# Performance work log

Measured on AMD Instinct MI355X. Metric: run time of the kernel, lower is better.

## Reference

```python
import jax, jax.numpy as jnp
import numpy as np

S, D = 4096, 512


def setup_inputs() -> dict:
    key = jax.random.key(0)
    ks = jax.random.split(key, 10)
    names = ['x', 'w_ql', 'w_kl', 'w_qr', 'w_kr', 'w_qg', 'w_kg', 'w_qloc', 'w_kloc', 'w_v']
    shapes = [(S, D)] + [(D, D)] * 9
    scale = [1.0] + [float(np.sqrt(2.0 / (D + D)))] * 9  # xavier-ish for weights
    return {n: jax.random.normal(k, sh, dtype=jnp.float32) * s
            for n, k, sh, s in zip(names, ks, shapes, scale)}


def reference(x, w_ql, w_kl, w_qr, w_kr, w_qg, w_kg, w_qloc, w_kloc, w_v):
    # x: [S, D]
    s, d = x.shape
    norm = jnp.sqrt(jnp.asarray(d, x.dtype))
    # strict upper triangle (j > i) is masked for the left boundary,
    # strict lower triangle (i > j) for the right boundary
    mask_up = jnp.triu(jnp.ones((s, s), dtype=bool), k=1)

    ql, kl = x @ w_ql, x @ w_kl
    qr, kr = x @ w_qr, x @ w_kr

    neg_inf = jnp.asarray(-jnp.inf, x.dtype)
    left_scores = jnp.where(mask_up, neg_inf, ql @ kl.T) / norm            # [S,S]
    left_boundary = jax.nn.softmax(left_scores, axis=1)
    right_scores = jnp.where(mask_up.T, neg_inf, qr @ kr.T) / norm
    right_boundary = jax.nn.softmax(right_scores, axis=1)

    # left_boundary @ triu(ones)  == forward cumsum along columns
    # right_boundary @ tril(ones) == reverse cumsum along columns
    left_cdf = jnp.cumsum(left_boundary, axis=1)
    right_cdf = jnp.cumsum(right_boundary[:, ::-1], axis=1)[:, ::-1]
    att_mask = left_cdf * right_cdf                                        # [S,S]

    s_glb = (x @ w_qg) @ (x @ w_kg).T                                      # [S,S]
    s_loc = ((x @ w_qloc) @ (x @ w_kloc).T) * att_mask                     # additive local path
    score = (s_glb + s_loc) / norm

    att_weight = jax.nn.softmax(score, axis=1)
    att_output = att_weight @ (x @ w_v)                                    # [S,D]
    return att_output, att_weight
```

## Files before the change

### kernel.cpp

```cpp
#include <hip/hip_runtime.h>


#define SS 4096
#define DD 512
#define INV_NORM 0.04419417382415922f

typedef _Float16 f16;
typedef f16 f16x8 __attribute__((ext_vector_type(8)));
typedef f16 f16x4 __attribute__((ext_vector_type(4)));
typedef float f32x4 __attribute__((ext_vector_type(4)));

#define GAS __attribute__((address_space(1)))
#define LAS __attribute__((address_space(3)))

__device__ __forceinline__ void ldsdma16(const void* g, void* l) {
  __builtin_amdgcn_global_load_lds((const GAS void*)g, (LAS void*)l, 16, 0, 0);
}

__device__ __forceinline__ void stage16(const f16* __restrict__ src, int ldk, f16* lds, int k0) {
  const int tid  = threadIdx.x;
  const int lane = tid & 63;
  const int wv   = tid >> 6;
  const int rb   = wv * 8 + (lane >> 3);
  const int cs   = lane & 7;
#pragma unroll
  for (int c = 0; c < 4; ++c) {
    const int r = c * 32 + rb;
    const int q = cs ^ (r & 7);
    ldsdma16(src + (size_t)r * ldk + k0 + q * 8, lds + c * 2048 + wv * 512);
  }
}

__device__ __forceinline__ f16x8 fragld(const f16* lds, int r0, int qb) {
  const int lane = threadIdx.x & 63;
  const int r = r0 + (lane & 15);
  const int q = (qb + (lane >> 4)) ^ (r & 7);
  return *(const f16x8*)(lds + r * 64 + q * 8);
}

__device__ __forceinline__ void mma64(const f16* As, const f16* Bs, f32x4 acc[2][8]) {
  const int wv = threadIdx.x >> 6;
#pragma unroll
  for (int ks = 0; ks < 2; ++ks) {
    const f16x8 a0 = fragld(As, wv * 32,      ks * 4);
    const f16x8 a1 = fragld(As, wv * 32 + 16, ks * 4);
#pragma unroll
    for (int j = 0; j < 8; ++j) {
      const f16x8 b = fragld(Bs, j * 16, ks * 4);
      acc[0][j] = __builtin_amdgcn_mfma_f32_16x16x32_f16(a0, b, acc[0][j], 0, 0, 0);
      acc[1][j] = __builtin_amdgcn_mfma_f32_16x16x32_f16(a1, b, acc[1][j], 0, 0, 0);
    }
  }
}

__global__ void k_cvt_x(const float* __restrict__ x, f16* __restrict__ xh) {
  const size_t i = ((size_t)blockIdx.x * 256 + threadIdx.x) * 4;
  const float4 f = *(const float4*)(x + i);
  f16x4 h = { (f16)f.x, (f16)f.y, (f16)f.z, (f16)f.w };
  *(f16x4*)(xh + i) = h;
}

__global__ void k_trw(const float* w0, const float* w1, const float* w2, const float* w3,
                      const float* w4, const float* w5, const float* w6, const float* w7,
                      const float* w8, f16* __restrict__ wt) {
  const float* srcs[9] = {w0, w1, w2, w3, w4, w5, w6, w7, w8};
  const float* src = srcs[blockIdx.z];
  f16* dst = wt + (size_t)blockIdx.z * DD * DD;
  __shared__ float t[32][33];
  const int n0 = blockIdx.x * 32, k0 = blockIdx.y * 32;
  const int tx = threadIdx.x, ty = threadIdx.y;
#pragma unroll
  for (int i = 0; i < 32; i += 8)
    t[ty + i][tx] = src[(size_t)(k0 + ty + i) * DD + n0 + tx];
  __syncthreads();
#pragma unroll
  for (int i = 0; i < 32; i += 8)
    dst[(size_t)(n0 + ty + i) * DD + k0 + tx] = (f16)t[tx][ty + i];
}

__global__ void k_trv(const f16* __restrict__ v, f16* __restrict__ vt) {
  __shared__ f16 t[32][33];
  const int n0 = blockIdx.x * 32, s0 = blockIdx.y * 32;
  const int tx = threadIdx.x, ty = threadIdx.y;
#pragma unroll
  for (int i = 0; i < 32; i += 8)
    t[ty + i][tx] = v[(size_t)(s0 + ty + i) * DD + n0 + tx];
  __syncthreads();
#pragma unroll
  for (int i = 0; i < 32; i += 8)
    vt[(size_t)(n0 + ty + i) * SS + s0 + tx] = t[tx][ty + i];
}

__global__ __launch_bounds__(256, 2) void k_proj(const f16* __restrict__ xh,
                                                 const f16* __restrict__ wt,
                                                 f16* __restrict__ proj) {
  __shared__ __align__(16) f16 As[8192];
  __shared__ __align__(16) f16 Bs[8192];
  const int z = blockIdx.z;
  const f16* B = wt + (size_t)z * DD * DD;
  f16* C = proj + (size_t)z * SS * DD;
  const int R0 = blockIdx.y * 128, C0 = blockIdx.x * 128;
  f32x4 acc[2][8];
#pragma unroll
  for (int i = 0; i < 2; ++i)
#pragma unroll
    for (int j = 0; j < 8; ++j) acc[i][j] = (f32x4){0.f, 0.f, 0.f, 0.f};
  for (int kb = 0; kb < DD / 64; ++kb) {
    __syncthreads();
    stage16(xh + (size_t)R0 * DD, DD, As, kb * 64);
    stage16(B  + (size_t)C0 * DD, DD, Bs, kb * 64);
    __syncthreads();
    mma64(As, Bs, acc);
  }
  const int lane = threadIdx.x & 63, wv = threadIdx.x >> 6;
  const int mm = lane & 15, quad = lane >> 4;
#pragma unroll
  for (int i = 0; i < 2; ++i)
#pragma unroll
    for (int j = 0; j < 8; ++j)
#pragma unroll
      for (int r = 0; r < 4; ++r)
        C[(size_t)(R0 + wv * 32 + i * 16 + quad * 4 + r) * DD + C0 + j * 16 + mm] =
            (f16)acc[i][j][r];
}

__global__ __launch_bounds__(256, 2) void k_bnd(const f16* __restrict__ proj,
                                                f16* __restrict__ eL,
                                                f16* __restrict__ eR) {
  const int jt = blockIdx.x, rbk = blockIdx.y, dir = blockIdx.z;
  if (dir == 0 ? (jt > rbk) : (jt < rbk)) return;
  __shared__ __align__(16) f16 As[8192];
  __shared__ __align__(16) f16 Bs[8192];
  const f16* q  = proj + (size_t)(dir ? 2 : 0) * SS * DD;
  const f16* kp = proj + (size_t)(dir ? 3 : 1) * SS * DD;
  const int R0 = rbk * 128, C0 = jt * 128;
  f32x4 acc[2][8];
#pragma unroll
  for (int i = 0; i < 2; ++i)
#pragma unroll
    for (int j = 0; j < 8; ++j) acc[i][j] = (f32x4){0.f, 0.f, 0.f, 0.f};
  for (int kb = 0; kb < DD / 64; ++kb) {
    __syncthreads();
    stage16(q  + (size_t)R0 * DD, DD, As, kb * 64);
    stage16(kp + (size_t)C0 * DD, DD, Bs, kb * 64);
    __syncthreads();
    mma64(As, Bs, acc);
  }
  const int lane = threadIdx.x & 63, wv = threadIdx.x >> 6;
  const int mm = lane & 15, quad = lane >> 4;
  const bool diag = (jt == rbk);
  f16* outp = dir ? eR : eL;
#pragma unroll
  for (int i = 0; i < 2; ++i)
#pragma unroll
    for (int r = 0; r < 4; ++r) {
      const int rl = wv * 32 + i * 16 + quad * 4 + r;
#pragma unroll
      for (int j = 0; j < 8; ++j) {
        const int cl = j * 16 + mm;
        const float sc = acc[i][j][r] * INV_NORM;
        const bool bad = diag && (dir ? (cl < rl) : (cl > rl));
        const float e = bad ? 0.f : __expf(sc);
        outp[(size_t)(R0 + rl) * SS + (C0 + cl)] = (f16)e;
      }
    }
}

__global__ __launch_bounds__(1024) void k_cumsum(f16* __restrict__ eL,
                                                 const f16* __restrict__ eR) {
  const int i = blockIdx.x;
  const int tid = threadIdx.x, lane = tid & 63, wv = tid >> 6;
  __shared__ float wsL[16], wsR[16];
  const int j0 = tid * 4;

  const f16x4 hl = *(const f16x4*)(eL + (size_t)i * SS + j0);
  float pl[4];
#pragma unroll
  for (int u = 0; u < 4; ++u) pl[u] = (j0 + u <= i) ? (float)hl[u] : 0.f;
#pragma unroll
  for (int u = 1; u < 4; ++u) pl[u] += pl[u - 1];
  const float Tl = pl[3];
  float sl = Tl;
#pragma unroll
  for (int d = 1; d < 64; d <<= 1) {
    const float o = __shfl_up(sl, (unsigned)d, 64);
    if (lane >= d) sl += o;
  }
  if (lane == 63) wsL[wv] = sl;

  const f16x4 hr = *(const f16x4*)(eR + (size_t)i * SS + j0);
  float rr[4], pr[4];
#pragma unroll
  for (int u = 0; u < 4; ++u) rr[u] = (j0 + u >= i) ? (float)hr[u] : 0.f;
  pr[0] = rr[0];
#pragma unroll
  for (int u = 1; u < 4; ++u) pr[u] = pr[u - 1] + rr[u];
  const float Tr = pr[3];
  float sr = Tr;
#pragma unroll
  for (int d = 1; d < 64; d <<= 1) {
    const float o = __shfl_up(sr, (unsigned)d, 64);
    if (lane >= d) sr += o;
  }
  if (lane == 63) wsR[wv] = sr;

  __syncthreads();
  float offL = 0.f, totL = 0.f, offR = 0.f, totR = 0.f;
#pragma unroll
  for (int ww = 0; ww < 16; ++ww) {
    const float a = wsL[ww], b = wsR[ww];
    if (ww < wv) { offL += a; offR += b; }
    totL += a; totR += b;
  }
  const float exL = offL + sl - Tl;
  const float exR = offR + sr - Tr;
  const float invL = 1.f / totL, invR = 1.f / totR;

  f16x4 out;
#pragma unroll
  for (int u = 0; u < 4; ++u) {
    const int j = j0 + u;
    const float cdfL = (exL + pl[u]) * invL;
    const float pre  = exR + pr[u];
    const float cdfR = (totR - pre + rr[u]) * invR;
    const float m = (j < i) ? cdfL : ((j > i) ? cdfR : 1.f);
    out[u] = (f16)m;
  }
  *(f16x4*)(eL + (size_t)i * SS + j0) = out;
}

__global__ __launch_bounds__(256, 2) void k_score(const f16* __restrict__ proj,
                                                  const f16* __restrict__ mask,
                                                  f16* __restrict__ ehalf,
                                                  float* __restrict__ lsc) {
  __shared__ __align__(16) f16 Ag[8192];
  __shared__ __align__(16) f16 Bg[8192];
  __shared__ __align__(16) f16 Al[8192];
  __shared__ __align__(16) f16 Bl[8192];
  const int jt = blockIdx.x, rbk = blockIdx.y;
  const f16* qg = proj + (size_t)4 * SS * DD;
  const f16* kg = proj + (size_t)5 * SS * DD;
  const f16* ql = proj + (size_t)6 * SS * DD;
  const f16* kl = proj + (size_t)7 * SS * DD;
  const int R0 = rbk * 128, C0 = jt * 128;
  f32x4 ag[2][8], al[2][8];
#pragma unroll
  for (int i = 0; i < 2; ++i)
#pragma unroll
    for (int j = 0; j < 8; ++j) {
      ag[i][j] = (f32x4){0.f, 0.f, 0.f, 0.f};
      al[i][j] = (f32x4){0.f, 0.f, 0.f, 0.f};
    }
  for (int kb = 0; kb < DD / 64; ++kb) {
    __syncthreads();
    stage16(qg + (size_t)R0 * DD, DD, Ag, kb * 64);
    stage16(kg + (size_t)C0 * DD, DD, Bg, kb * 64);
    stage16(ql + (size_t)R0 * DD, DD, Al, kb * 64);
    stage16(kl + (size_t)C0 * DD, DD, Bl, kb * 64);
    __syncthreads();
    mma64(Ag, Bg, ag);
    mma64(Al, Bl, al);
  }
  const int lane = threadIdx.x & 63, wv = threadIdx.x >> 6;
  const int mm = lane & 15, quad = lane >> 4;
  float ls[2][4];
#pragma unroll
  for (int i = 0; i < 2; ++i)
#pragma unroll
    for (int r = 0; r < 4; ++r) ls[i][r] = 0.f;
#pragma unroll
  for (int i = 0; i < 2; ++i)
#pragma unroll
    for (int r = 0; r < 4; ++r) {
      const int rg = R0 + wv * 32 + i * 16 + quad * 4 + r;
#pragma unroll
      for (int j = 0; j < 8; ++j) {
        const int cg = C0 + j * 16 + mm;
        const float mk = (float)mask[(size_t)rg * SS + cg];
        const float scv = (ag[i][j][r] + al[i][j][r] * mk) * INV_NORM;
        const float e = __expf(scv);
        ehalf[(size_t)rg * SS + cg] = (f16)e;
        ls[i][r] += e;
      }
    }
#pragma unroll
  for (int d = 1; d < 16; d <<= 1)
#pragma unroll
    for (int i = 0; i < 2; ++i)
#pragma unroll
      for (int r = 0; r < 4; ++r)
        ls[i][r] += __shfl_xor(ls[i][r], d, 64);
  if (mm == 0) {
#pragma unroll
    for (int i = 0; i < 2; ++i)
#pragma unroll
      for (int r = 0; r < 4; ++r)
        atomicAdd(&lsc[R0 + wv * 32 + i * 16 + quad * 4 + r], ls[i][r]);
  }
}

__global__ void k_norm(const f16* __restrict__ ehalf, const float* __restrict__ lsc,
                       float* __restrict__ outw) {
  const size_t idx = ((size_t)blockIdx.x * 256 + threadIdx.x) * 8;
  const int row = (int)(idx >> 12);
  const float inv = 1.f / lsc[row];
  const f16x8 h = *(const f16x8*)(ehalf + idx);
  float4 a = { (float)h[0] * inv, (float)h[1] * inv, (float)h[2] * inv, (float)h[3] * inv };
  float4 b = { (float)h[4] * inv, (float)h[5] * inv, (float)h[6] * inv, (float)h[7] * inv };
  *(float4*)(outw + idx) = a;
  *(float4*)(outw + idx + 4) = b;
}

__global__ __launch_bounds__(256, 2) void k_pv(const f16* __restrict__ ehalf,
                                               const f16* __restrict__ vt,
                                               float* __restrict__ part) {
  __shared__ __align__(16) f16 As[8192];
  __shared__ __align__(16) f16 Bs[8192];
  const int C0 = blockIdx.x * 128, R0 = blockIdx.y * 128, zk = blockIdx.z;
  f32x4 acc[2][8];
#pragma unroll
  for (int i = 0; i < 2; ++i)
#pragma unroll
    for (int j = 0; j < 8; ++j) acc[i][j] = (f32x4){0.f, 0.f, 0.f, 0.f};
  for (int kb = 0; kb < 16; ++kb) {
    const int k0 = zk * 1024 + kb * 64;
    __syncthreads();
    stage16(ehalf + (size_t)R0 * SS, SS, As, k0);
    stage16(vt    + (size_t)C0 * SS, SS, Bs, k0);
    __syncthreads();
    mma64(As, Bs, acc);
  }
  const int lane = threadIdx.x & 63, wv = threadIdx.x >> 6;
  const int mm = lane & 15, quad = lane >> 4;
  float* P = part + (size_t)zk * SS * DD;
#pragma unroll
  for (int i = 0; i < 2; ++i)
#pragma unroll
    for (int j = 0; j < 8; ++j)
#pragma unroll
      for (int r = 0; r < 4; ++r)
        P[(size_t)(R0 + wv * 32 + i * 16 + quad * 4 + r) * DD + C0 + j * 16 + mm] =
            acc[i][j][r];
}

__global__ void k_red(const float* __restrict__ part, const float* __restrict__ lsc,
                      float* __restrict__ O) {
  const size_t idx = ((size_t)blockIdx.x * 256 + threadIdx.x) * 4;
  const int row = (int)(idx >> 9);
  float4 s = {0.f, 0.f, 0.f, 0.f};
#pragma unroll
  for (int p = 0; p < 4; ++p) {
    const float4 v = *(const float4*)(part + (size_t)p * SS * DD + idx);
    s.x += v.x; s.y += v.y; s.z += v.z; s.w += v.w;
  }
  const float inv = 1.f / lsc[row];
  s.x *= inv; s.y *= inv; s.z *= inv; s.w *= inv;
  *(float4*)(O + idx) = s;
}

extern "C" void kernel_launch(void* const* d_in, const int* in_sizes, int n_in,
                              void* d_out, int out_size, void* d_ws, size_t ws_size,
                              hipStream_t stream) {
  (void)in_sizes; (void)n_in; (void)out_size; (void)ws_size;
  const float* x = (const float*)d_in[0];
  const float* w[9];
  for (int i = 0; i < 9; ++i) w[i] = (const float*)d_in[1 + i];
  float* O    = (float*)d_out;
  float* outw = O + (size_t)SS * DD;

  char* ws = (char*)d_ws;
  size_t off = 0;
  auto alloc = [&](size_t b) { void* p = ws + off; off += (b + 255) & ~(size_t)255; return p; };
  f16* xh     = (f16*)alloc((size_t)SS * DD * 2);
  f16* wt     = (f16*)alloc((size_t)9 * DD * DD * 2);
  f16* proj   = (f16*)alloc((size_t)9 * SS * DD * 2);
  f16* vt     = (f16*)alloc((size_t)DD * SS * 2);
  f16* eL     = (f16*)alloc((size_t)SS * SS * 2);
  f16* eR     = (f16*)alloc((size_t)SS * SS * 2);
  f16* ehalf  = (f16*)alloc((size_t)SS * SS * 2);
  float* lsc  = (float*)alloc((size_t)SS * 4);
  float* part = (float*)eR;

  hipMemsetAsync(lsc, 0, (size_t)SS * 4, stream);
  k_cvt_x<<<SS * DD / 1024, 256, 0, stream>>>(x, xh);
  k_trw<<<dim3(16, 16, 9), dim3(32, 8), 0, stream>>>(w[0], w[1], w[2], w[3], w[4],
                                                     w[5], w[6], w[7], w[8], wt);
  k_proj<<<dim3(4, 32, 9), 256, 0, stream>>>(xh, wt, proj);
  k_trv<<<dim3(16, 128), dim3(32, 8), 0, stream>>>(proj + (size_t)8 * SS * DD, vt);
  k_bnd<<<dim3(32, 32, 2), 256, 0, stream>>>(proj, eL, eR);
  k_cumsum<<<SS, 1024, 0, stream>>>(eL, eR);
  k_score<<<dim3(32, 32), 256, 0, stream>>>(proj, eL, ehalf, lsc);
  k_norm<<<SS * SS / 2048, 256, 0, stream>>>(ehalf, lsc, outw);
  k_pv<<<dim3(4, 32, 4), 256, 0, stream>>>(ehalf, vt, part);
  k_red<<<SS * DD / 1024, 256, 0, stream>>>(part, lsc, O);
}
```

Measured before the change: 306.1 us.

## Compact triangular boundary grid, skip masked loads, bf16 partials, fuse norm and reduce

Launches the boundary kernel over only the needed triangular tiles instead of exiting early, and skips loading masked-off halves of rows in the cumsum kernel. PV split-K partials are stored as bf16 to halve their write and read traffic. The normalization and partial-reduction kernels are merged into one launch. The bf16 partials add rounding error to the output.

```diff
diff --git a/kernel.cpp b/kernel.cpp
--- a/kernel.cpp
+++ b/kernel.cpp
@@ -9,12 +9,22 @@
 typedef f16 f16x8 __attribute__((ext_vector_type(8)));
 typedef f16 f16x4 __attribute__((ext_vector_type(4)));
 typedef float f32x4 __attribute__((ext_vector_type(4)));
+typedef unsigned short ushort;
+typedef ushort ushort4v __attribute__((ext_vector_type(4)));
 
 #define GAS __attribute__((address_space(1)))
 #define LAS __attribute__((address_space(3)))
 
 __device__ __forceinline__ void ldsdma16(const void* g, void* l) {
   __builtin_amdgcn_global_load_lds((const GAS void*)g, (LAS void*)l, 16, 0, 0);
+}
+
+__device__ __forceinline__ ushort f2bf(float f) {
+  unsigned u = __float_as_uint(f);
+  return (ushort)((u + 0x7FFFu + ((u >> 16) & 1u)) >> 16);
+}
+__device__ __forceinline__ float bf2f(ushort h) {
+  return __uint_as_float((unsigned)h << 16);
 }
 
 __device__ __forceinline__ void stage16(const f16* __restrict__ src, int ldk, f16* lds, int k0) {
@@ -127,8 +137,12 @@
 __global__ __launch_bounds__(256, 2) void k_bnd(const f16* __restrict__ proj,
                                                 f16* __restrict__ eL,
                                                 f16* __restrict__ eR) {
-  const int jt = blockIdx.x, rbk = blockIdx.y, dir = blockIdx.z;
-  if (dir == 0 ? (jt > rbk) : (jt < rbk)) return;
+  const int t = blockIdx.x, dir = blockIdx.y;
+  int rbk = (int)((sqrtf(8.f * t + 1.f) - 1.f) * 0.5f);
+  while ((rbk + 1) * (rbk + 2) / 2 <= t) ++rbk;
+  while (rbk * (rbk + 1) / 2 > t) --rbk;
+  int jt = t - rbk * (rbk + 1) / 2;
+  if (dir) { jt = 31 - jt; rbk = 31 - rbk; }
   __shared__ __align__(16) f16 As[8192];
   __shared__ __align__(16) f16 Bs[8192];
   const f16* q  = proj + (size_t)(dir ? 2 : 0) * SS * DD;
@@ -173,10 +187,12 @@
   __shared__ float wsL[16], wsR[16];
   const int j0 = tid * 4;
 
-  const f16x4 hl = *(const f16x4*)(eL + (size_t)i * SS + j0);
-  float pl[4];
-#pragma unroll
-  for (int u = 0; u < 4; ++u) pl[u] = (j0 + u <= i) ? (float)hl[u] : 0.f;
+  float pl[4] = {0.f, 0.f, 0.f, 0.f};
+  if (j0 <= i) {
+    const f16x4 hl = *(const f16x4*)(eL + (size_t)i * SS + j0);
+#pragma unroll
+    for (int u = 0; u < 4; ++u) pl[u] = (j0 + u <= i) ? (float)hl[u] : 0.f;
+  }
 #pragma unroll
   for (int u = 1; u < 4; ++u) pl[u] += pl[u - 1];
   const float Tl = pl[3];
@@ -188,10 +204,12 @@
   }
   if (lane == 63) wsL[wv] = sl;
 
-  const f16x4 hr = *(const f16x4*)(eR + (size_t)i * SS + j0);
-  float rr[4], pr[4];
-#pragma unroll
-  for (int u = 0; u < 4; ++u) rr[u] = (j0 + u >= i) ? (float)hr[u] : 0.f;
+  float rr[4] = {0.f, 0.f, 0.f, 0.f}, pr[4];
+  if (j0 + 3 >= i) {
+    const f16x4 hr = *(const f16x4*)(eR + (size_t)i * SS + j0);
+#pragma unroll
+    for (int u = 0; u < 4; ++u) rr[u] = (j0 + u >= i) ? (float)hr[u] : 0.f;
+  }
   pr[0] = rr[0];
 #pragma unroll
   for (int u = 1; u < 4; ++u) pr[u] = pr[u - 1] + rr[u];
@@ -299,21 +317,9 @@
   }
 }
 
-__global__ void k_norm(const f16* __restrict__ ehalf, const float* __restrict__ lsc,
-                       float* __restrict__ outw) {
-  const size_t idx = ((size_t)blockIdx.x * 256 + threadIdx.x) * 8;
-  const int row = (int)(idx >> 12);
-  const float inv = 1.f / lsc[row];
-  const f16x8 h = *(const f16x8*)(ehalf + idx);
-  float4 a = { (float)h[0] * inv, (float)h[1] * inv, (float)h[2] * inv, (float)h[3] * inv };
-  float4 b = { (float)h[4] * inv, (float)h[5] * inv, (float)h[6] * inv, (float)h[7] * inv };
-  *(float4*)(outw + idx) = a;
-  *(float4*)(outw + idx + 4) = b;
-}
-
 __global__ __launch_bounds__(256, 2) void k_pv(const f16* __restrict__ ehalf,
                                                const f16* __restrict__ vt,
-                                               float* __restrict__ part) {
+                                               ushort* __restrict__ part) {
   __shared__ __align__(16) f16 As[8192];
   __shared__ __align__(16) f16 Bs[8192];
   const int C0 = blockIdx.x * 128, R0 = blockIdx.y * 128, zk = blockIdx.z;
@@ -332,7 +338,7 @@
   }
   const int lane = threadIdx.x & 63, wv = threadIdx.x >> 6;
   const int mm = lane & 15, quad = lane >> 4;
-  float* P = part + (size_t)zk * SS * DD;
+  ushort* P = part + (size_t)zk * SS * DD;
 #pragma unroll
   for (int i = 0; i < 2; ++i)
 #pragma unroll
@@ -340,22 +346,35 @@
 #pragma unroll
       for (int r = 0; r < 4; ++r)
         P[(size_t)(R0 + wv * 32 + i * 16 + quad * 4 + r) * DD + C0 + j * 16 + mm] =
-            acc[i][j][r];
-}
-
-__global__ void k_red(const float* __restrict__ part, const float* __restrict__ lsc,
+            f2bf(acc[i][j][r]);
+}
+
+__global__ void k_fin(const f16* __restrict__ ehalf, const ushort* __restrict__ part,
+                      const float* __restrict__ lsc, float* __restrict__ outw,
                       float* __restrict__ O) {
-  const size_t idx = ((size_t)blockIdx.x * 256 + threadIdx.x) * 4;
-  const int row = (int)(idx >> 9);
-  float4 s = {0.f, 0.f, 0.f, 0.f};
-#pragma unroll
-  for (int p = 0; p < 4; ++p) {
-    const float4 v = *(const float4*)(part + (size_t)p * SS * DD + idx);
-    s.x += v.x; s.y += v.y; s.z += v.z; s.w += v.w;
-  }
-  const float inv = 1.f / lsc[row];
-  s.x *= inv; s.y *= inv; s.z *= inv; s.w *= inv;
-  *(float4*)(O + idx) = s;
+  const int bx = blockIdx.x;
+  if (bx < 8192) {
+    const size_t idx = ((size_t)bx * 256 + threadIdx.x) * 8;
+    const int row = (int)(idx >> 12);
+    const float inv = 1.f / lsc[row];
+    const f16x8 h = *(const f16x8*)(ehalf + idx);
+    float4 a = { (float)h[0] * inv, (float)h[1] * inv, (float)h[2] * inv, (float)h[3] * inv };
+    float4 b = { (float)h[4] * inv, (float)h[5] * inv, (float)h[6] * inv, (float)h[7] * inv };
+    *(float4*)(outw + idx) = a;
+    *(float4*)(outw + idx + 4) = b;
+  } else {
+    const size_t idx = ((size_t)(bx - 8192) * 256 + threadIdx.x) * 4;
+    const int row = (int)(idx >> 9);
+    float s0 = 0.f, s1 = 0.f, s2 = 0.f, s3 = 0.f;
+#pragma unroll
+    for (int p = 0; p < 4; ++p) {
+      const ushort4v v = *(const ushort4v*)(part + (size_t)p * SS * DD + idx);
+      s0 += bf2f(v[0]); s1 += bf2f(v[1]); s2 += bf2f(v[2]); s3 += bf2f(v[3]);
+    }
+    const float inv = 1.f / lsc[row];
+    float4 s = { s0 * inv, s1 * inv, s2 * inv, s3 * inv };
+    *(float4*)(O + idx) = s;
+  }
 }
 
 extern "C" void kernel_launch(void* const* d_in, const int* in_sizes, int n_in,
@@ -379,7 +398,7 @@
   f16* eR     = (f16*)alloc((size_t)SS * SS * 2);
   f16* ehalf  = (f16*)alloc((size_t)SS * SS * 2);
   float* lsc  = (float*)alloc((size_t)SS * 4);
-  float* part = (float*)eR;
+  ushort* part = (ushort*)eR;
 
   hipMemsetAsync(lsc, 0, (size_t)SS * 4, stream);
   k_cvt_x<<<SS * DD / 1024, 256, 0, stream>>>(x, xh);
@@ -387,10 +406,9 @@
                                                      w[5], w[6], w[7], w[8], wt);
   k_proj<<<dim3(4, 32, 9), 256, 0, stream>>>(xh, wt, proj);
   k_trv<<<dim3(16, 128), dim3(32, 8), 0, stream>>>(proj + (size_t)8 * SS * DD, vt);
-  k_bnd<<<dim3(32, 32, 2), 256, 0, stream>>>(proj, eL, eR);
+  k_bnd<<<dim3(528, 2), 256, 0, stream>>>(proj, eL, eR);
   k_cumsum<<<SS, 1024, 0, stream>>>(eL, eR);
   k_score<<<dim3(32, 32), 256, 0, stream>>>(proj, eL, ehalf, lsc);
-  k_norm<<<SS * SS / 2048, 256, 0, stream>>>(ehalf, lsc, outw);
   k_pv<<<dim3(4, 32, 4), 256, 0, stream>>>(ehalf, vt, part);
-  k_red<<<SS * DD / 1024, 256, 0, stream>>>(part, lsc, O);
-}
+  k_fin<<<10240, 256, 0, stream>>>(ehalf, part, lsc, outw, O);
+}
```

New measurement: 295.3 us. 1.04x faster.
